# Optimization experiments

Measured on AMD Instinct MI355X. Metric: run time of the kernel, lower is better.

## Reference

```python
import jax, jax.numpy as jnp
import numpy as np

# Module hyperparameters (from init_kwargs)
KH, KW = 3, 3        # kernel_size
SH, SW = 1, 1        # stride
PH, PW = 1, 1        # padding
NUM_ITER = 3         # num_iterations


def squash(t, axis=-1):
    # scale = |t|^2 / (1 + |t|^2); out = scale * t / |t|
    sq = jnp.sum(t * t, axis=axis, keepdims=True)
    return (sq / (1.0 + sq)) * t / jnp.sqrt(sq)


def setup_inputs() -> dict:
    key = jax.random.key(0)
    k1, k2 = jax.random.split(key)
    x = jax.random.normal(k1, (4, 32, 56, 56), dtype=jnp.float32)
    # weight: (P_out, P_in, K, L_in, L_out) = (64//16, 32//8, 3*3, 8, 16)
    # (the original stores an extra size-1 dim at position 2; squeezed here)
    weight = jax.random.normal(k2, (4, 4, 9, 8, 16), dtype=jnp.float32)
    return {"x": x, "weight": weight}


def reference(x, weight):
    N, C_in, H, W = x.shape
    P_out, P_in, K, L_in, L_out = weight.shape
    H_out = (H + 2 * PH - KH) // SH + 1
    W_out = (W + 2 * PW - KW) // SW + 1

    # im2col: (N, C_in, H_out, W_out, K)
    xp = jnp.pad(x, ((0, 0), (0, 0), (PH, PH), (PW, PW)))
    patches = jnp.stack(
        [xp[:, :, dj:dj + SH * H_out:SH, dk:dk + SW * W_out:SW]
         for dj in range(KH) for dk in range(KW)],
        axis=-1,
    )
    # split channels into capsule planes: (N, P_in, L_in, H_out, W_out, K)
    patches = patches.reshape(N, P_in, L_in, H_out, W_out, K)

    # priors[n,o,p,h,w,k,:] = window[n,p,h,w,k,:] @ weight[o,p,k,:,:]
    priors = jnp.einsum('nplhwk,opkld->nophwkd', patches, weight)

    # dynamic routing. logits broadcast over the L_out dim in the original
    # (delta_logits has a keepdim size-1 last axis), so track them as (...,K,1).
    logits = jnp.zeros(priors.shape[:-1] + (1,), priors.dtype)
    outputs = None
    for i in range(NUM_ITER):
        probs = jax.nn.softmax(logits, axis=-2)          # softmax over K
        s = jnp.sum(probs * priors, axis=-2, keepdims=True)  # (...,1,L_out)
        outputs = squash(s, axis=-1)
        if i != NUM_ITER - 1:
            logits = logits + jnp.sum(priors * outputs, axis=-1, keepdims=True)

    # sum routed outputs over input capsule planes (the .add accumulation)
    out = jnp.sum(outputs[..., 0, :], axis=2)            # (N, P_out, H_out, W_out, L_out)
    out = jnp.transpose(out, (0, 1, 4, 2, 3)).reshape(N, P_out * L_out, H_out, W_out)
    return out
```

## Files before the change

### kernel.cpp

```cpp
#include <hip/hip_runtime.h>


#define HW 56
#define HW2 3136
#define WSTRIDE 1168

__global__ void caps_routing_kernel(
    const float* __restrict__ x, const float* __restrict__ wgt,
    float* __restrict__ out)
{
    __shared__ float lds_w[4 * WSTRIDE];

    const int tid = threadIdx.x;
    const int bx  = blockIdx.x;
    const int n = bx >> 2, o = bx & 3;

    {
        const float4* wsrc = (const float4*)(wgt + o * 4608);
        for (int i = tid; i < 1152; i += 256) {
            const int pp  = i / 288;
            const int rem = i - pp * 288;
            *(float4*)&lds_w[pp * WSTRIDE + rem * 4] = wsrc[i];
        }
    }
    __syncthreads();

    const int wl = tid & 3;
    const int dq = (tid >> 2) & 3;
    const int p  = (tid >> 4) & 3;

    const int t  = blockIdx.y * 4 + (tid >> 6);
    const int h  = t / 14;
    const int w0 = (t - h * 14) * 4;

    float M[9][4];
    #pragma unroll
    for (int k = 0; k < 9; ++k)
        #pragma unroll
        for (int j = 0; j < 4; ++j) M[k][j] = 0.f;

    const float* xp = x + (n * 32 + p * 8) * HW2;
    const float* wbase = &lds_w[p * WSTRIDE + dq * 4];
    const int colbase = w0 + wl - 1;

    #pragma clang loop unroll(disable)
    for (int l = 0; l < 8; ++l) {
        #pragma unroll
        for (int rr = 0; rr < 3; ++rr) {
            const int row = h + rr - 1;
            const bool rv = (unsigned)row < (unsigned)HW;
            const float* xrow = xp + l * HW2 + row * HW;
            float xv[3];
            #pragma unroll
            for (int c = 0; c < 3; ++c) {
                const int col = colbase + c;
                xv[c] = (rv && (unsigned)col < (unsigned)HW) ? xrow[col] : 0.f;
            }
            #pragma unroll
            for (int kc = 0; kc < 3; ++kc) {
                const int k = rr * 3 + kc;
                const float4 wa = *(const float4*)(wbase + (k * 8 + l) * 16);
                const float xs = xv[kc];
                M[k][0] += xs * wa.x; M[k][1] += xs * wa.y;
                M[k][2] += xs * wa.z; M[k][3] += xs * wa.w;
            }
        }
    }

    float v[4], b[9];
    {
        float s[4];
        #pragma unroll
        for (int j = 0; j < 4; ++j) {
            float a = M[0][j];
            #pragma unroll
            for (int k = 1; k < 9; ++k) a += M[k][j];
            s[j] = a * (1.f / 9.f);
        }
        float sq = s[0]*s[0] + s[1]*s[1] + s[2]*s[2] + s[3]*s[3];
        sq += __shfl_xor(sq, 4, 64);
        sq += __shfl_xor(sq, 8, 64);
        const float scale = sq * __builtin_amdgcn_rsqf(sq) * __builtin_amdgcn_rcpf(1.f + sq);
        #pragma unroll
        for (int j = 0; j < 4; ++j) v[j] = s[j] * scale;
        #pragma unroll
        for (int k = 0; k < 9; ++k) {
            float u = M[k][0]*v[0] + M[k][1]*v[1] + M[k][2]*v[2] + M[k][3]*v[3];
            u += __shfl_xor(u, 4, 64);
            u += __shfl_xor(u, 8, 64);
            b[k] = u;
        }
    }

    #pragma unroll
    for (int it = 1; it < 3; ++it) {
        float mx = b[0];
        #pragma unroll
        for (int k = 1; k < 9; ++k) mx = fmaxf(mx, b[k]);
        float e[9]; float se = 0.f;
        #pragma unroll
        for (int k = 0; k < 9; ++k) { e[k] = __expf(b[k] - mx); se += e[k]; }
        const float inv = __builtin_amdgcn_rcpf(se);
        float s[4];
        #pragma unroll
        for (int j = 0; j < 4; ++j) {
            float a = 0.f;
            #pragma unroll
            for (int k = 0; k < 9; ++k) a += e[k] * M[k][j];
            s[j] = a * inv;
        }
        float sq = s[0]*s[0] + s[1]*s[1] + s[2]*s[2] + s[3]*s[3];
        sq += __shfl_xor(sq, 4, 64);
        sq += __shfl_xor(sq, 8, 64);
        const float scale = sq * __builtin_amdgcn_rsqf(sq) * __builtin_amdgcn_rcpf(1.f + sq);
        #pragma unroll
        for (int j = 0; j < 4; ++j) v[j] = s[j] * scale;
        if (it == 1) {
            #pragma unroll
            for (int k = 0; k < 9; ++k) {
                float u = M[k][0]*v[0] + M[k][1]*v[1] + M[k][2]*v[2] + M[k][3]*v[3];
                u += __shfl_xor(u, 4, 64);
                u += __shfl_xor(u, 8, 64);
                b[k] += u;
            }
        }
    }

    #pragma unroll
    for (int j = 0; j < 4; ++j) {
        v[j] += __shfl_xor(v[j], 16, 64);
        v[j] += __shfl_xor(v[j], 32, 64);
    }
    if (p == 0) {
        float* op = out + ((n * 64 + o * 16 + dq * 4) * HW + h) * HW + w0 + wl;
        #pragma unroll
        for (int j = 0; j < 4; ++j) op[j * HW2] = v[j];
    }
}

extern "C" void kernel_launch(void* const* d_in, const int* in_sizes, int n_in,
                              void* d_out, int out_size, void* d_ws, size_t ws_size,
                              hipStream_t stream) {
    const float* x   = (const float*)d_in[0];
    const float* wgt = (const float*)d_in[1];
    float* out = (float*)d_out;

    caps_routing_kernel<<<dim3(16, 196), dim3(256), 0, stream>>>(x, wgt, out);
}
```

Baseline: 82.08 us.

## Compute two output rows per thread to reuse input rows and weight loads

Each thread now handles two adjacent output rows. It loads four input rows per capsule plane instead of three per single row, and reuses each LDS weight float4 for both rows. The grid's y dimension is halved, which cuts redundant global loads, LDS weight reads and the per-block weight staging. In exchange the accumulator array doubles to 72 floats, raising register pressure and possibly lowering occupancy. The grid becomes 16x98 blocks, which still fills the device.

```diff
diff --git a/kernel.cpp b/kernel.cpp
--- a/kernel.cpp
+++ b/kernel.cpp
@@ -30,14 +30,15 @@
     const int p  = (tid >> 4) & 3;
 
     const int t  = blockIdx.y * 4 + (tid >> 6);
-    const int h  = t / 14;
-    const int w0 = (t - h * 14) * 4;
+    const int hp = t / 14;
+    const int w0 = (t - hp * 14) * 4;
+    const int h0 = hp * 2;
 
-    float M[9][4];
+    float M[9][4][2];
     #pragma unroll
     for (int k = 0; k < 9; ++k)
         #pragma unroll
-        for (int j = 0; j < 4; ++j) M[k][j] = 0.f;
+        for (int j = 0; j < 4; ++j) { M[k][j][0] = 0.f; M[k][j][1] = 0.f; }
 
     const float* xp = x + (n * 32 + p * 8) * HW2;
     const float* wbase = &lds_w[p * WSTRIDE + dq * 4];
@@ -45,96 +46,108 @@
 
     #pragma clang loop unroll(disable)
     for (int l = 0; l < 8; ++l) {
+        float xv[4][3];
+        const float* xplane = xp + l * HW2;
         #pragma unroll
-        for (int rr = 0; rr < 3; ++rr) {
-            const int row = h + rr - 1;
+        for (int rr = 0; rr < 4; ++rr) {
+            const int row = h0 + rr - 1;
             const bool rv = (unsigned)row < (unsigned)HW;
-            const float* xrow = xp + l * HW2 + row * HW;
-            float xv[3];
+            const float* xrow = xplane + row * HW;
             #pragma unroll
             for (int c = 0; c < 3; ++c) {
                 const int col = colbase + c;
-                xv[c] = (rv && (unsigned)col < (unsigned)HW) ? xrow[col] : 0.f;
+                xv[rr][c] = (rv && (unsigned)col < (unsigned)HW) ? xrow[col] : 0.f;
             }
+        }
+        #pragma unroll
+        for (int rr = 0; rr < 3; ++rr) {
             #pragma unroll
             for (int kc = 0; kc < 3; ++kc) {
                 const int k = rr * 3 + kc;
                 const float4 wa = *(const float4*)(wbase + (k * 8 + l) * 16);
-                const float xs = xv[kc];
-                M[k][0] += xs * wa.x; M[k][1] += xs * wa.y;
-                M[k][2] += xs * wa.z; M[k][3] += xs * wa.w;
-            }
-        }
-    }
-
-    float v[4], b[9];
-    {
-        float s[4];
-        #pragma unroll
-        for (int j = 0; j < 4; ++j) {
-            float a = M[0][j];
-            #pragma unroll
-            for (int k = 1; k < 9; ++k) a += M[k][j];
-            s[j] = a * (1.f / 9.f);
-        }
-        float sq = s[0]*s[0] + s[1]*s[1] + s[2]*s[2] + s[3]*s[3];
-        sq += __shfl_xor(sq, 4, 64);
-        sq += __shfl_xor(sq, 8, 64);
-        const float scale = sq * __builtin_amdgcn_rsqf(sq) * __builtin_amdgcn_rcpf(1.f + sq);
-        #pragma unroll
-        for (int j = 0; j < 4; ++j) v[j] = s[j] * scale;
-        #pragma unroll
-        for (int k = 0; k < 9; ++k) {
-            float u = M[k][0]*v[0] + M[k][1]*v[1] + M[k][2]*v[2] + M[k][3]*v[3];
-            u += __shfl_xor(u, 4, 64);
-            u += __shfl_xor(u, 8, 64);
-            b[k] = u;
-        }
-    }
-
-    #pragma unroll
-    for (int it = 1; it < 3; ++it) {
-        float mx = b[0];
-        #pragma unroll
-        for (int k = 1; k < 9; ++k) mx = fmaxf(mx, b[k]);
-        float e[9]; float se = 0.f;
-        #pragma unroll
-        for (int k = 0; k < 9; ++k) { e[k] = __expf(b[k] - mx); se += e[k]; }
-        const float inv = __builtin_amdgcn_rcpf(se);
-        float s[4];
-        #pragma unroll
-        for (int j = 0; j < 4; ++j) {
-            float a = 0.f;
-            #pragma unroll
-            for (int k = 0; k < 9; ++k) a += e[k] * M[k][j];
-            s[j] = a * inv;
-        }
-        float sq = s[0]*s[0] + s[1]*s[1] + s[2]*s[2] + s[3]*s[3];
-        sq += __shfl_xor(sq, 4, 64);
-        sq += __shfl_xor(sq, 8, 64);
-        const float scale = sq * __builtin_amdgcn_rsqf(sq) * __builtin_amdgcn_rcpf(1.f + sq);
-        #pragma unroll
-        for (int j = 0; j < 4; ++j) v[j] = s[j] * scale;
-        if (it == 1) {
-            #pragma unroll
-            for (int k = 0; k < 9; ++k) {
-                float u = M[k][0]*v[0] + M[k][1]*v[1] + M[k][2]*v[2] + M[k][3]*v[3];
-                u += __shfl_xor(u, 4, 64);
-                u += __shfl_xor(u, 8, 64);
-                b[k] += u;
+                const float xs0 = xv[rr][kc];
+                const float xs1 = xv[rr + 1][kc];
+                M[k][0][0] += xs0 * wa.x; M[k][1][0] += xs0 * wa.y;
+                M[k][2][0] += xs0 * wa.z; M[k][3][0] += xs0 * wa.w;
+                M[k][0][1] += xs1 * wa.x; M[k][1][1] += xs1 * wa.y;
+                M[k][2][1] += xs1 * wa.z; M[k][3][1] += xs1 * wa.w;
             }
         }
     }
 
     #pragma unroll
-    for (int j = 0; j < 4; ++j) {
-        v[j] += __shfl_xor(v[j], 16, 64);
-        v[j] += __shfl_xor(v[j], 32, 64);
-    }
-    if (p == 0) {
-        float* op = out + ((n * 64 + o * 16 + dq * 4) * HW + h) * HW + w0 + wl;
+    for (int ti = 0; ti < 2; ++ti) {
+        float v[4], b[9];
+        {
+            float s[4];
+            #pragma unroll
+            for (int j = 0; j < 4; ++j) {
+                float a = M[0][j][ti];
+                #pragma unroll
+                for (int k = 1; k < 9; ++k) a += M[k][j][ti];
+                s[j] = a * (1.f / 9.f);
+            }
+            float sq = s[0]*s[0] + s[1]*s[1] + s[2]*s[2] + s[3]*s[3];
+            sq += __shfl_xor(sq, 4, 64);
+            sq += __shfl_xor(sq, 8, 64);
+            const float scale = sq * __builtin_amdgcn_rsqf(sq) * __builtin_amdgcn_rcpf(1.f + sq);
+            #pragma unroll
+            for (int j = 0; j < 4; ++j) v[j] = s[j] * scale;
+            #pragma unroll
+            for (int k = 0; k < 9; ++k) {
+                float u = M[k][0][ti]*v[0] + M[k][1][ti]*v[1]
+                        + M[k][2][ti]*v[2] + M[k][3][ti]*v[3];
+                u += __shfl_xor(u, 4, 64);
+                u += __shfl_xor(u, 8, 64);
+                b[k] = u;
+            }
+        }
+
         #pragma unroll
-        for (int j = 0; j < 4; ++j) op[j * HW2] = v[j];
+        for (int it = 1; it < 3; ++it) {
+            float mx = b[0];
+            #pragma unroll
+            for (int k = 1; k < 9; ++k) mx = fmaxf(mx, b[k]);
+            float e[9]; float se = 0.f;
+            #pragma unroll
+            for (int k = 0; k < 9; ++k) { e[k] = __expf(b[k] - mx); se += e[k]; }
+            const float inv = __builtin_amdgcn_rcpf(se);
+            float s[4];
+            #pragma unroll
+            for (int j = 0; j < 4; ++j) {
+                float a = 0.f;
+                #pragma unroll
+                for (int k = 0; k < 9; ++k) a += e[k] * M[k][j][ti];
+                s[j] = a * inv;
+            }
+            float sq = s[0]*s[0] + s[1]*s[1] + s[2]*s[2] + s[3]*s[3];
+            sq += __shfl_xor(sq, 4, 64);
+            sq += __shfl_xor(sq, 8, 64);
+            const float scale = sq * __builtin_amdgcn_rsqf(sq) * __builtin_amdgcn_rcpf(1.f + sq);
+            #pragma unroll
+            for (int j = 0; j < 4; ++j) v[j] = s[j] * scale;
+            if (it == 1) {
+                #pragma unroll
+                for (int k = 0; k < 9; ++k) {
+                    float u = M[k][0][ti]*v[0] + M[k][1][ti]*v[1]
+                            + M[k][2][ti]*v[2] + M[k][3][ti]*v[3];
+                    u += __shfl_xor(u, 4, 64);
+                    u += __shfl_xor(u, 8, 64);
+                    b[k] += u;
+                }
+            }
+        }
+
+        #pragma unroll
+        for (int j = 0; j < 4; ++j) {
+            v[j] += __shfl_xor(v[j], 16, 64);
+            v[j] += __shfl_xor(v[j], 32, 64);
+        }
+        if (p == 0) {
+            float* op = out + ((n * 64 + o * 16 + dq * 4) * HW + (h0 + ti)) * HW + w0 + wl;
+            #pragma unroll
+            for (int j = 0; j < 4; ++j) op[j * HW2] = v[j];
+        }
     }
 }
 
@@ -145,5 +158,5 @@
     const float* wgt = (const float*)d_in[1];
     float* out = (float*)d_out;
 
-    caps_routing_kernel<<<dim3(16, 196), dim3(256), 0, stream>>>(x, wgt, out);
+    caps_routing_kernel<<<dim3(16, 98), dim3(256), 0, stream>>>(x, wgt, out);
 }
```

Result: faster. 77.94 us (-5.0%).
